# Optimization experiments

Hardware: AMD Instinct MI355X
Metric: run time of the kernel (lower is better)

Reference implementation:

```python
import jax, jax.numpy as jnp
import numpy as np

N_NODES = 100000
N_EDGES = 1600000
IN_F, HID_F, OUT_F = 128, 128, 128


def setup_inputs() -> dict:
    key = jax.random.key(0)
    k1, k2, k3, k4, k5, k6 = jax.random.split(key, 6)
    x = jax.random.normal(k1, (N_NODES, IN_F), dtype=jnp.float32)
    edge_index = jax.random.randint(k2, (2, N_EDGES), 0, N_NODES, dtype=jnp.int32)
    # nn.Linear params (PyTorch layout: W [out, in], y = x @ W.T + b)
    s1 = 1.0 / np.sqrt(IN_F)
    W1 = jax.random.uniform(k3, (HID_F, IN_F), minval=-s1, maxval=s1, dtype=jnp.float32)
    b1 = jax.random.uniform(k4, (HID_F,), minval=-s1, maxval=s1, dtype=jnp.float32)
    s2 = 1.0 / np.sqrt(HID_F)
    W2 = jax.random.uniform(k5, (OUT_F, HID_F), minval=-s2, maxval=s2, dtype=jnp.float32)
    b2 = jax.random.uniform(k6, (OUT_F,), minval=-s2, maxval=s2, dtype=jnp.float32)
    return {"x": x, "edge_index": edge_index, "W1": W1, "b1": b1, "W2": W2, "b2": b2}


def _spmm_mean(h, row, col, deg_inv):
    # (adj @ h)[i] = sum_{edges e: row[e]==i} h[col[e]], then scale by deg_inv[i]
    agg = jax.ops.segment_sum(h[col], row, num_segments=N_NODES)
    return agg * deg_inv[:, None]


def reference(x, edge_index, W1, b1, W2, b2):
    row, col = edge_index[0], edge_index[1]
    # degree = row-sum of adjacency (duplicates in COO are summed, matching torch)
    deg = jax.ops.segment_sum(jnp.ones((N_EDGES,), dtype=x.dtype), row, num_segments=N_NODES)
    deg_inv = jnp.where(deg > 0, 1.0 / deg, 0.0)
    # dropout in eval mode = identity
    h = x @ W1.T + b1
    h = _spmm_mean(h, row, col, deg_inv)
    h = jax.nn.elu(h)
    h = h @ W2.T + b2
    h = _spmm_mean(h, row, col, deg_inv)
    return h
```

## Files before the change

kernel.cpp:

```cpp
#include <hip/hip_runtime.h>
#include <math.h>

#define N_NODES 100000
#define N_EDGES 1600000
#define F 128
#define NBUCK 391
#define EPB 4096
#define CAP 4800

#define XCH512 (N_NODES * F / 8 / 512)
#define WCH512 (F * F / 2 / 512)

typedef _Float16 f16x2 __attribute__((ext_vector_type(2)));
typedef _Float16 f16x8 __attribute__((ext_vector_type(8)));
typedef __fp16 fp16x2 __attribute__((ext_vector_type(2)));
typedef float f32x2 __attribute__((ext_vector_type(2)));
typedef float f32x4 __attribute__((ext_vector_type(4)));

__device__ inline uint pkrtz(float a, float b) {
    union { fp16x2 h; uint u; } c;
    c.h = __builtin_amdgcn_cvt_pkrtz(a, b);
    return c.u;
}
__device__ inline f16x2 as2(uint u) {
    union { uint u; f16x2 h; } c; c.u = u; return c.h;
}

__device__ inline int wave_incl_scan(int v, int lane) {
#pragma unroll
    for (int off = 1; off < 64; off <<= 1) {
        int t = __shfl_up(v, off);
        if (lane >= off) v += t;
    }
    return v;
}


__global__ __launch_bounds__(512) void build_convert_kernel(
        const int* __restrict__ row, const int* __restrict__ col,
        int* __restrict__ bucket_cursor, int* __restrict__ pairs,
        const float* __restrict__ X, const float* __restrict__ W1,
        const float* __restrict__ W2, uint* __restrict__ Xh,
        uint* __restrict__ W1h, uint* __restrict__ W2h) {
    __shared__ int stage[EPB];
    __shared__ ushort bid[EPB];
    __shared__ int lcnt[NBUCK], lcur[NBUCK], loff[NBUCK], gbase[NBUCK];
    __shared__ int wsum[8];
    const int blk = blockIdx.x;
    const int tid = threadIdx.x;

    if (blk >= NBUCK) {
        if (blk < NBUCK + XCH512) {
            int i = (blk - NBUCK) * 512 + tid;
            float4 a = *(const float4*)&X[(size_t)i * 8];
            float4 c = *(const float4*)&X[(size_t)i * 8 + 4];
            uint4 o = {pkrtz(a.x, a.y), pkrtz(a.z, a.w), pkrtz(c.x, c.y), pkrtz(c.z, c.w)};
            *(uint4*)&Xh[(size_t)i * 4] = o;
        } else {
            int i = (blk - NBUCK - XCH512) * 512 + tid;
            float2 a = *(const float2*)&W1[i * 2];
            float2 c = *(const float2*)&W2[i * 2];
            W1h[i] = pkrtz(a.x, a.y);
            W2h[i] = pkrtz(c.x, c.y);
        }
        return;
    }

    const int lane = tid & 63;
    const int wid = tid >> 6;
    const int base = blk * EPB;
    const int cnt = min(N_EDGES - base, EPB);

    for (int i = tid; i < NBUCK; i += 512) { lcnt[i] = 0; lcur[i] = 0; }
    __syncthreads();
    for (int i = 0; i < EPB / 512; ++i) {
        int e = base + i * 512 + tid;
        if (e < N_EDGES) atomicAdd(&lcnt[row[e] >> 8], 1);
    }
    __syncthreads();
    {
        int v = (tid < NBUCK) ? lcnt[tid] : 0;
        int inc = wave_incl_scan(v, lane);
        if (lane == 63) wsum[wid] = inc;
        __syncthreads();
        if (tid == 0) {
            int a = 0;
#pragma unroll
            for (int i = 0; i < 8; ++i) { int t = wsum[i]; wsum[i] = a; a += t; }
        }
        __syncthreads();
        if (tid < NBUCK) loff[tid] = inc - v + wsum[wid];
    }
    if (tid < NBUCK) {
        int c = lcnt[tid];
        gbase[tid] = c ? atomicAdd(&bucket_cursor[tid], c) : 0;
    }
    __syncthreads();
    for (int i = 0; i < EPB / 512; ++i) {
        int e = base + i * 512 + tid;
        if (e < N_EDGES) {
            int r = row[e], c = col[e];
            int b = r >> 8;
            int rk = atomicAdd(&lcur[b], 1);
            int q = loff[b] + rk;
            stage[q] = ((r & 255) << 17) | c;
            bid[q] = (ushort)b;
        }
    }
    __syncthreads();
    for (int q = tid; q < cnt; q += 512) {
        int b = bid[q];
        int t = gbase[b] + (q - loff[b]);
        if (t < CAP) pairs[b * CAP + t] = stage[q];
    }
}

__global__ __launch_bounds__(1024) void csr_finalize_kernel(const int* __restrict__ pairs,
                                                            const int* __restrict__ bucket_cursor,
                                                            int* __restrict__ csr_col,
                                                            int2* __restrict__ rs,
                                                            float* __restrict__ deg_inv) {
    __shared__ int rcnt[256], rcnt2[256], roff[256];
    __shared__ int colstage[CAP];
    __shared__ int wsum[4];
    const int tid = threadIdx.x;
    const int lane = tid & 63;
    const int wid = tid >> 6;
    const int b = blockIdx.x;
    const int cnt = min(bucket_cursor[b], CAP);
    const int base = b * CAP;
    const int* reg = &pairs[base];

    if (tid < 256) { rcnt[tid] = 0; rcnt2[tid] = 0; }
    __syncthreads();
    for (int q = tid; q < cnt; q += 1024) atomicAdd(&rcnt[reg[q] >> 17], 1);
    __syncthreads();
    int d = 0, inc = 0;
    if (tid < 256) {
        d = rcnt[tid];
        inc = wave_incl_scan(d, lane);
        if (lane == 63) wsum[wid] = inc;
    }
    __syncthreads();
    if (tid == 0) {
        int a = 0;
#pragma unroll
        for (int i = 0; i < 4; ++i) { int t = wsum[i]; wsum[i] = a; a += t; }
    }
    __syncthreads();
    if (tid < 256) {
        const int excl = inc - d + wsum[wid];
        roff[tid] = excl;
        const int grow = (b << 8) + tid;
        if (grow < N_NODES) {
            rs[grow] = make_int2(base + excl, d);
            deg_inv[grow] = d ? 1.0f / (float)d : 0.0f;
        }
    }
    __syncthreads();
    for (int q = tid; q < cnt; q += 1024) {
        int v = reg[q];
        int lr = v >> 17;
        int rk = atomicAdd(&rcnt2[lr], 1);
        colstage[roff[lr] + rk] = v & 0x1FFFF;
    }
    __syncthreads();
    for (int q = tid; q < cnt; q += 1024) csr_col[base + q] = colstage[q];
}


template <bool ELU, bool OUT_F32>
__global__ __launch_bounds__(256, 6) void fused_agg_gemm_kernel(
        const ushort* __restrict__ H,
        const int2* __restrict__ rs,
        const int* __restrict__ csr_col,
        const float* __restrict__ deg_inv,
        const ushort* __restrict__ Wh,
        const float* __restrict__ bias,
        void* __restrict__ out) {
    __shared__ __align__(16) ushort xs[16 * 136];

    const int tid = threadIdx.x;
    const int m0 = blockIdx.x << 4;
    const int g = tid >> 4;
    const int fo = (tid & 15) << 3;

    {
        const int node = m0 + g;
        f32x2 a[4];
#pragma unroll
        for (int i = 0; i < 4; ++i) a[i] = (f32x2){0.f, 0.f};
        const int2 sd = rs[node];
        int p = sd.x;
        const int e = sd.x + sd.y;
        const float di = deg_inv[node];
        if (p + 7 < e) {
            int cc[8];
#pragma unroll
            for (int k = 0; k < 8; ++k) cc[k] = __builtin_nontemporal_load(&csr_col[p + k]);
            while (true) {
                uint4 vv[8];
#pragma unroll
                for (int k = 0; k < 8; ++k) vv[k] = *(const uint4*)&H[(size_t)cc[k] * F + fo];
                p += 8;
                const bool more = (p + 7 < e);
                int cn[8];
                if (more) {
#pragma unroll
                    for (int k = 0; k < 8; ++k) cn[k] = __builtin_nontemporal_load(&csr_col[p + k]);
                }
                asm volatile("" :: "v"(vv[0].x), "v"(vv[1].x), "v"(vv[2].x), "v"(vv[3].x),
                                   "v"(vv[4].x), "v"(vv[5].x), "v"(vv[6].x), "v"(vv[7].x));
#pragma unroll
                for (int k = 0; k < 8; k += 4) {
                    f16x2 h0 = (as2(vv[k].x) + as2(vv[k + 1].x)) + (as2(vv[k + 2].x) + as2(vv[k + 3].x));
                    f16x2 h1 = (as2(vv[k].y) + as2(vv[k + 1].y)) + (as2(vv[k + 2].y) + as2(vv[k + 3].y));
                    f16x2 h2 = (as2(vv[k].z) + as2(vv[k + 1].z)) + (as2(vv[k + 2].z) + as2(vv[k + 3].z));
                    f16x2 h3 = (as2(vv[k].w) + as2(vv[k + 1].w)) + (as2(vv[k + 2].w) + as2(vv[k + 3].w));
                    a[0] += (f32x2){(float)h0.x, (float)h0.y};
                    a[1] += (f32x2){(float)h1.x, (float)h1.y};
                    a[2] += (f32x2){(float)h2.x, (float)h2.y};
                    a[3] += (f32x2){(float)h3.x, (float)h3.y};
                }
                if (!more) break;
#pragma unroll
                for (int k = 0; k < 8; ++k) cc[k] = cn[k];
            }
        }
        if (p + 3 < e) {
            int c0 = csr_col[p], c1 = csr_col[p + 1], c2 = csr_col[p + 2], c3 = csr_col[p + 3];
            uint4 v0 = *(const uint4*)&H[(size_t)c0 * F + fo];
            uint4 v1 = *(const uint4*)&H[(size_t)c1 * F + fo];
            uint4 v2 = *(const uint4*)&H[(size_t)c2 * F + fo];
            uint4 v3 = *(const uint4*)&H[(size_t)c3 * F + fo];
            f16x2 h0 = (as2(v0.x) + as2(v1.x)) + (as2(v2.x) + as2(v3.x));
            f16x2 h1 = (as2(v0.y) + as2(v1.y)) + (as2(v2.y) + as2(v3.y));
            f16x2 h2 = (as2(v0.z) + as2(v1.z)) + (as2(v2.z) + as2(v3.z));
            f16x2 h3 = (as2(v0.w) + as2(v1.w)) + (as2(v2.w) + as2(v3.w));
            a[0] += (f32x2){(float)h0.x, (float)h0.y};
            a[1] += (f32x2){(float)h1.x, (float)h1.y};
            a[2] += (f32x2){(float)h2.x, (float)h2.y};
            a[3] += (f32x2){(float)h3.x, (float)h3.y};
            p += 4;
        }
        if (p + 1 < e) {
            int c0 = csr_col[p], c1 = csr_col[p + 1];
            uint4 v0 = *(const uint4*)&H[(size_t)c0 * F + fo];
            uint4 v1 = *(const uint4*)&H[(size_t)c1 * F + fo];
            f16x2 h0 = as2(v0.x) + as2(v1.x);
            f16x2 h1 = as2(v0.y) + as2(v1.y);
            f16x2 h2 = as2(v0.z) + as2(v1.z);
            f16x2 h3 = as2(v0.w) + as2(v1.w);
            a[0] += (f32x2){(float)h0.x, (float)h0.y};
            a[1] += (f32x2){(float)h1.x, (float)h1.y};
            a[2] += (f32x2){(float)h2.x, (float)h2.y};
            a[3] += (f32x2){(float)h3.x, (float)h3.y};
            p += 2;
        }
        if (p < e) {
            int c = csr_col[p];
            uint4 v = *(const uint4*)&H[(size_t)c * F + fo];
            f16x2 h0 = as2(v.x), h1 = as2(v.y), h2 = as2(v.z), h3 = as2(v.w);
            a[0] += (f32x2){(float)h0.x, (float)h0.y};
            a[1] += (f32x2){(float)h1.x, (float)h1.y};
            a[2] += (f32x2){(float)h2.x, (float)h2.y};
            a[3] += (f32x2){(float)h3.x, (float)h3.y};
        }
        uint4 o = {pkrtz(a[0].x * di, a[0].y * di), pkrtz(a[1].x * di, a[1].y * di),
                   pkrtz(a[2].x * di, a[2].y * di), pkrtz(a[3].x * di, a[3].y * di)};
        *(uint4*)&xs[g * 136 + fo] = o;
    }
    __syncthreads();

    const int w = tid >> 6;
    const int lane = tid & 63;
    const int q = lane >> 4;
    const int t = lane & 15;

    f16x8 xfr[4];
#pragma unroll
    for (int kk = 0; kk < 4; ++kk)
        xfr[kk] = *(const f16x8*)&xs[t * 136 + kk * 32 + q * 8];

    if (!OUT_F32) __syncthreads();

    const int node = m0 + t;
    const float dv = deg_inv[node];
    const float mk = (dv > 0.f) ? 1.f : 0.f;

    f32x4 vout[2];
#pragma unroll
    for (int jj = 0; jj < 2; ++jj) {
        const int j = (w << 1) | jj;
        f32x4 acc = (f32x4){0.f, 0.f, 0.f, 0.f};
        const ushort* wrow = &Wh[(j * 16 + t) * F + q * 8];
#pragma unroll
        for (int kk = 0; kk < 4; ++kk) {
            f16x8 wfr = *(const f16x8*)&wrow[kk * 32];
            acc = __builtin_amdgcn_mfma_f32_16x16x32_f16(wfr, xfr[kk], acc, 0, 0, 0);
        }
        f32x4 bb = *(const f32x4*)&bias[j * 16 + q * 4];
        f32x4 v = acc + bb * mk;
        if (ELU) {
#pragma unroll
            for (int r = 0; r < 4; ++r) v[r] = (v[r] > 0.f) ? v[r] : expm1f(v[r]);
        }
        vout[jj] = v;
    }

    if (OUT_F32) {
        float* of = &((float*)out)[(size_t)node * F + (w << 5) + q * 4];
        __builtin_nontemporal_store(vout[0], (f32x4*)of);
        __builtin_nontemporal_store(vout[1], (f32x4*)(of + 16));
    } else {
        ushort* ys = xs;
        uint2 o0 = {pkrtz(vout[0][0], vout[0][1]), pkrtz(vout[0][2], vout[0][3])};
        uint2 o1 = {pkrtz(vout[1][0], vout[1][1]), pkrtz(vout[1][2], vout[1][3])};
        *(uint2*)&ys[t * 136 + (w << 5) + q * 4] = o0;
        *(uint2*)&ys[t * 136 + (w << 5) + 16 + q * 4] = o1;
        __syncthreads();
        const int n2 = tid >> 4, seg = tid & 15;
        uint4 vo = *(const uint4*)&ys[n2 * 136 + seg * 8];
        __builtin_nontemporal_store(*(f32x4*)&vo,
            (f32x4*)&((ushort*)out)[(size_t)(m0 + n2) * F + seg * 8]);
    }
}


extern "C" void kernel_launch(void* const* d_in, const int* in_sizes, int n_in,
                              void* d_out, int out_size, void* d_ws, size_t ws_size,
                              hipStream_t stream) {
    const float* x  = (const float*)d_in[0];
    const int*   ei = (const int*)d_in[1];
    const float* W1 = (const float*)d_in[2];
    const float* b1 = (const float*)d_in[3];
    const float* W2 = (const float*)d_in[4];
    const float* b2 = (const float*)d_in[5];
    float* out = (float*)d_out;

    const int* row = ei;
    const int* col = ei + N_EDGES;

    ushort* bufA = (ushort*)d_ws;
    ushort* bufB = bufA + (size_t)N_NODES * F;
    int* csr_col = (int*)(bufB + (size_t)N_NODES * F);
    int2* rs = (int2*)(csr_col + NBUCK * CAP);
    float* deg_inv = (float*)(rs + N_NODES + 4);
    int* bucket_cursor = (int*)(deg_inv + N_NODES);
    uint* W1h = (uint*)(bucket_cursor + 512);
    uint* W2h = W1h + F * F / 2;
    int* pairs = (int*)bufA;

    (void)hipMemsetAsync(bucket_cursor, 0, 512 * sizeof(int), stream);
    build_convert_kernel<<<NBUCK + XCH512 + WCH512, 512, 0, stream>>>(
        row, col, bucket_cursor, pairs, x, W1, W2, (uint*)bufB, W1h, W2h);
    csr_finalize_kernel<<<NBUCK, 1024, 0, stream>>>(pairs, bucket_cursor, csr_col, rs, deg_inv);

    const int fb = N_NODES / 16;
    fused_agg_gemm_kernel<true, false><<<fb, 256, 0, stream>>>(
        (const ushort*)bufB, rs, csr_col, deg_inv, (const ushort*)W1h, b1, bufA);
    fused_agg_gemm_kernel<false, true><<<fb, 256, 0, stream>>>(
        bufA, rs, csr_col, deg_inv, (const ushort*)W2h, b2, out);
}
```

Before: 274.5 us.

## Sort nodes by degree within buckets to balance aggregation work per wave

```diff
diff --git a/kernel.cpp b/kernel.cpp
--- a/kernel.cpp
+++ b/kernel.cpp
@@ -119,10 +119,12 @@
                                                             const int* __restrict__ bucket_cursor,
                                                             int* __restrict__ csr_col,
                                                             int2* __restrict__ rs,
-                                                            float* __restrict__ deg_inv) {
+                                                            float* __restrict__ deg_inv,
+                                                            int* __restrict__ perm) {
     __shared__ int rcnt[256], rcnt2[256], roff[256];
     __shared__ int colstage[CAP];
     __shared__ int wsum[4];
+    __shared__ int hist[64], hcur[64], hoff[64];
     const int tid = threadIdx.x;
     const int lane = tid & 63;
     const int wid = tid >> 6;
@@ -132,30 +134,40 @@
     const int* reg = &pairs[base];
 
     if (tid < 256) { rcnt[tid] = 0; rcnt2[tid] = 0; }
+    if (tid < 64) { hist[tid] = 0; hcur[tid] = 0; }
     __syncthreads();
     for (int q = tid; q < cnt; q += 1024) atomicAdd(&rcnt[reg[q] >> 17], 1);
     __syncthreads();
-    int d = 0, inc = 0;
+    int d = 0, inc = 0, bin = 63;
+    const int grow = (b << 8) + tid;
     if (tid < 256) {
         d = rcnt[tid];
         inc = wave_incl_scan(d, lane);
         if (lane == 63) wsum[wid] = inc;
+        bin = (grow < N_NODES) ? min(d, 62) : 63;
+        atomicAdd(&hist[bin], 1);
     }
     __syncthreads();
     if (tid == 0) {
         int a = 0;
 #pragma unroll
         for (int i = 0; i < 4; ++i) { int t = wsum[i]; wsum[i] = a; a += t; }
+    }
+    if (tid < 64) {
+        int v = hist[tid];
+        int hi = wave_incl_scan(v, tid);
+        hoff[tid] = hi - v;
     }
     __syncthreads();
     if (tid < 256) {
         const int excl = inc - d + wsum[wid];
         roff[tid] = excl;
-        const int grow = (b << 8) + tid;
         if (grow < N_NODES) {
             rs[grow] = make_int2(base + excl, d);
             deg_inv[grow] = d ? 1.0f / (float)d : 0.0f;
         }
+        int rank = hoff[bin] + atomicAdd(&hcur[bin], 1);
+        perm[(b << 8) + rank] = grow;
     }
     __syncthreads();
     for (int q = tid; q < cnt; q += 1024) {
@@ -175,6 +187,7 @@
         const int2* __restrict__ rs,
         const int* __restrict__ csr_col,
         const float* __restrict__ deg_inv,
+        const int* __restrict__ perm,
         const ushort* __restrict__ Wh,
         const float* __restrict__ bias,
         void* __restrict__ out) {
@@ -184,16 +197,16 @@
     const int m0 = blockIdx.x << 4;
     const int g = tid >> 4;
     const int fo = (tid & 15) << 3;
+    const int nodeA = perm[m0 + g];
 
     {
-        const int node = m0 + g;
         f32x2 a[4];
 #pragma unroll
         for (int i = 0; i < 4; ++i) a[i] = (f32x2){0.f, 0.f};
-        const int2 sd = rs[node];
+        const int2 sd = rs[nodeA];
         int p = sd.x;
         const int e = sd.x + sd.y;
-        const float di = deg_inv[node];
+        const float di = deg_inv[nodeA];
         if (p + 7 < e) {
             int cc[8];
 #pragma unroll
@@ -276,6 +289,7 @@
     const int lane = tid & 63;
     const int q = lane >> 4;
     const int t = lane & 15;
+    const int nodeB = perm[m0 + t];
 
     f16x8 xfr[4];
 #pragma unroll
@@ -284,8 +298,7 @@
 
     if (!OUT_F32) __syncthreads();
 
-    const int node = m0 + t;
-    const float dv = deg_inv[node];
+    const float dv = deg_inv[nodeB];
     const float mk = (dv > 0.f) ? 1.f : 0.f;
 
     f32x4 vout[2];
@@ -309,7 +322,7 @@
     }
 
     if (OUT_F32) {
-        float* of = &((float*)out)[(size_t)node * F + (w << 5) + q * 4];
+        float* of = &((float*)out)[(size_t)nodeB * F + (w << 5) + q * 4];
         __builtin_nontemporal_store(vout[0], (f32x4*)of);
         __builtin_nontemporal_store(vout[1], (f32x4*)(of + 16));
     } else {
@@ -322,7 +335,7 @@
         const int n2 = tid >> 4, seg = tid & 15;
         uint4 vo = *(const uint4*)&ys[n2 * 136 + seg * 8];
         __builtin_nontemporal_store(*(f32x4*)&vo,
-            (f32x4*)&((ushort*)out)[(size_t)(m0 + n2) * F + seg * 8]);
+            (f32x4*)&((ushort*)out)[(size_t)nodeA * F + seg * 8]);
     }
 }
 
@@ -346,7 +359,8 @@
     int* csr_col = (int*)(bufB + (size_t)N_NODES * F);
     int2* rs = (int2*)(csr_col + NBUCK * CAP);
     float* deg_inv = (float*)(rs + N_NODES + 4);
-    int* bucket_cursor = (int*)(deg_inv + N_NODES);
+    int* perm = (int*)(deg_inv + N_NODES);
+    int* bucket_cursor = perm + NBUCK * 256;
     uint* W1h = (uint*)(bucket_cursor + 512);
     uint* W2h = W1h + F * F / 2;
     int* pairs = (int*)bufA;
@@ -354,11 +368,11 @@
     (void)hipMemsetAsync(bucket_cursor, 0, 512 * sizeof(int), stream);
     build_convert_kernel<<<NBUCK + XCH512 + WCH512, 512, 0, stream>>>(
         row, col, bucket_cursor, pairs, x, W1, W2, (uint*)bufB, W1h, W2h);
-    csr_finalize_kernel<<<NBUCK, 1024, 0, stream>>>(pairs, bucket_cursor, csr_col, rs, deg_inv);
+    csr_finalize_kernel<<<NBUCK, 1024, 0, stream>>>(pairs, bucket_cursor, csr_col, rs, deg_inv, perm);
 
     const int fb = N_NODES / 16;
     fused_agg_gemm_kernel<true, false><<<fb, 256, 0, stream>>>(
-        (const ushort*)bufB, rs, csr_col, deg_inv, (const ushort*)W1h, b1, bufA);
+        (const ushort*)bufB, rs, csr_col, deg_inv, perm, (const ushort*)W1h, b1, bufA);
     fused_agg_gemm_kernel<false, true><<<fb, 256, 0, stream>>>(
-        bufA, rs, csr_col, deg_inv, (const ushort*)W2h, b2, out);
-}
+        bufA, rs, csr_col, deg_inv, perm, (const ushort*)W2h, b2, out);
+}
```

After: 301.2 us. 1.1x slower.
